# Kernel tuning notes

Hardware: AMD Instinct MI355X
Metric: run time of the kernel (lower is better)

Reference implementation:

```python
import jax, jax.numpy as jnp
import numpy as np

NUM_HEADS = 16
EMBED_DIM = 2048
HEAD_DIM = EMBED_DIM // NUM_HEADS        # 128
LATENT_DIM = HEAD_DIM // 4               # 32
GROUPS = HEAD_DIM // LATENT_DIM          # 4 latent sub-heads per q head
B, T = 1, 2048


def setup_inputs() -> dict:
    key = jax.random.key(0)
    ks = jax.random.split(key, 7)
    s_in = 1.0 / np.sqrt(EMBED_DIM)
    x = jax.random.normal(ks[0], (B, T, EMBED_DIM), dtype=jnp.float32)
    # torch Linear weights: [out_features, in_features]
    Wq = jax.random.normal(ks[1], (EMBED_DIM, EMBED_DIM), dtype=jnp.float32) * s_in
    Wk = jax.random.normal(ks[2], (EMBED_DIM, EMBED_DIM), dtype=jnp.float32) * s_in
    Wv = jax.random.normal(ks[3], (EMBED_DIM, EMBED_DIM), dtype=jnp.float32) * s_in
    Wlk = jax.random.normal(ks[4], (NUM_HEADS * LATENT_DIM, EMBED_DIM), dtype=jnp.float32) * s_in
    Wlv = jax.random.normal(ks[5], (NUM_HEADS * LATENT_DIM, EMBED_DIM), dtype=jnp.float32) * s_in
    Wo = jax.random.normal(ks[6], (EMBED_DIM, EMBED_DIM), dtype=jnp.float32) * s_in
    return {"x": x, "Wq": Wq, "Wk": Wk, "Wv": Wv, "Wlk": Wlk, "Wlv": Wlv, "Wo": Wo}


def reference(x, Wq, Wk, Wv, Wlk, Wlv, Wo):
    Bv, Tv, C = x.shape
    # q: [B,T,H,G,Dl]  (each head's 128-dim q split into 4 latent sub-heads)
    q = (x @ Wq.T).reshape(Bv, Tv, NUM_HEADS, GROUPS, LATENT_DIM)
    # latent k/v: [B,T,H,Dl], shared across the G sub-heads of each q head
    lk = (x @ Wlk.T).reshape(Bv, Tv, NUM_HEADS, LATENT_DIM)
    lv = (x @ Wlv.T).reshape(Bv, Tv, NUM_HEADS, LATENT_DIM)
    # k_proj / v_proj outputs are computed but unused in the original forward.
    scale = 1.0 / np.sqrt(HEAD_DIM).astype(np.float32)
    # scores: [B,H,G,T,T]
    scores = jnp.einsum('bthgd,bshd->bhgts', q, lk) * scale
    probs = jax.nn.softmax(scores, axis=-1)
    out = jnp.einsum('bhgts,bshd->bthgd', probs, lv).reshape(Bv, Tv, C)
    return out @ Wo.T
```

## Files before the change

kernel.cpp:

```cpp
#include <hip/hip_runtime.h>
#include <hip/hip_bf16.h>

typedef __bf16 bf16;
typedef __bf16 bf16x4 __attribute__((ext_vector_type(4)));
typedef __bf16 bf16x8 __attribute__((ext_vector_type(8)));
typedef float  f32x4  __attribute__((ext_vector_type(4)));

#define AS1 __attribute__((address_space(1)))
#define AS3 __attribute__((address_space(3)))

__device__ __forceinline__ void gload_lds16(const bf16* g, bf16* l) {
    __builtin_amdgcn_global_load_lds((const AS1 void*)g, (AS3 void*)l, 16, 0, 0);
}

__device__ __forceinline__ void stage8_f32(const float* s, bf16* l) {
    float4 a = *(const float4*)s;
    float4 b = *(const float4*)(s + 4);
    bf16x8 o;
    o[0] = (bf16)a.x; o[1] = (bf16)a.y; o[2] = (bf16)a.z; o[3] = (bf16)a.w;
    o[4] = (bf16)b.x; o[5] = (bf16)b.y; o[6] = (bf16)b.z; o[7] = (bf16)b.w;
    *(bf16x8*)l = o;
}

__device__ __forceinline__ void gemm_core64_k64(
    const bf16* __restrict__ A, const bf16* __restrict__ B,
    int m0, int n0, int K, f32x4 (&acc)[2][4],
    int wm, int r16, int q8)
{
    __shared__ __align__(16) bf16 As[2][128 * 64];
    __shared__ __align__(16) bf16 Bs[2][64 * 64];

    const int tid  = threadIdx.x;
    const int arow = tid >> 3;
    const int acol = ((tid & 7) ^ ((tid >> 3) & 7)) * 8;
    const int k7   = r16 & 7;

    auto stage = [&](int buf, int kt) {
#pragma unroll
        for (int j = 0; j < 4; ++j)
            gload_lds16(A + (size_t)(m0 + j * 32 + arow) * K + kt + acol,
                        &As[buf][(j * 256 + tid) * 8]);
#pragma unroll
        for (int j = 0; j < 2; ++j)
            gload_lds16(B + (size_t)(n0 + j * 32 + arow) * K + kt + acol,
                        &Bs[buf][(j * 256 + tid) * 8]);
    };

    stage(0, 0);
    __syncthreads();

    int cur = 0;
    for (int kt = 0; kt < K; kt += 64) {
        if (kt + 64 < K) stage(cur ^ 1, kt + 64);

        bf16x8 a[2][2], b[4][2];
#pragma unroll
        for (int r = 0; r < 2; ++r)
#pragma unroll
            for (int kc = 0; kc < 2; ++kc)
                a[r][kc] = *(const bf16x8*)&As[cur][(wm + r * 16 + r16) * 64
                                                   + ((kc * 4 + q8) ^ k7) * 8];
#pragma unroll
        for (int c = 0; c < 4; ++c)
#pragma unroll
            for (int kc = 0; kc < 2; ++kc)
                b[c][kc] = *(const bf16x8*)&Bs[cur][(c * 16 + r16) * 64
                                                   + ((kc * 4 + q8) ^ k7) * 8];
#pragma unroll
        for (int kc = 0; kc < 2; ++kc)
#pragma unroll
            for (int r = 0; r < 2; ++r)
#pragma unroll
                for (int c = 0; c < 4; ++c)
                    acc[r][c] = __builtin_amdgcn_mfma_f32_16x16x32_bf16(a[r][kc], b[c][kc], acc[r][c], 0, 0, 0);

        asm volatile("s_waitcnt vmcnt(0) lgkmcnt(0)" ::: "memory");
        __builtin_amdgcn_s_barrier();
        __builtin_amdgcn_sched_barrier(0);
        cur ^= 1;
    }
}

__global__ __launch_bounds__(256) void cvt4c(
    const float* __restrict__ s0, const float* __restrict__ s1,
    const float* __restrict__ s2, const float* __restrict__ s3,
    bf16* __restrict__ d0, bf16* __restrict__ d1, bf16* __restrict__ d2,
    bf16* __restrict__ d3)
{
    int bid = blockIdx.x;
    const float* S; bf16* D; int cb;
    if (bid < 2048)      { S = s0; D = d0; cb = bid; }
    else if (bid < 4096) { S = s1; D = d1; cb = bid - 2048; }
    else if (bid < 4608) { S = s2; D = d2; cb = bid - 4096; }
    else                 { S = s3; D = d3; cb = bid - 4608; }
    int off = (cb * 256 + threadIdx.x) * 8;
    stage8_f32(S + off, D + off);
}

__global__ __launch_bounds__(256) void proj_k64(
    const bf16* __restrict__ x, const bf16* __restrict__ Wq,
    const bf16* __restrict__ Wlk, const bf16* __restrict__ Wlv,
    bf16* __restrict__ Q, bf16* __restrict__ LK, bf16* __restrict__ LVt)
{
    const int hw  = blockIdx.x + 48 * blockIdx.y;
    const int xcd = hw & 7, c = hw >> 3;
    const int bx  = (xcd & 3) * 12 + c / 8;
    const int by  = (xcd >> 2) * 8 + (c & 7);

    const int tid = threadIdx.x, lane = tid & 63, wave = tid >> 6;
    const int wm = wave * 32;
    const int r16 = lane & 15, q8 = lane >> 4;
    f32x4 acc[2][4] = {};

    const bf16* Bv; int n0;
    if (bx < 32)      { Bv = Wq;  n0 = bx * 64; }
    else if (bx < 40) { Bv = Wlk; n0 = (bx - 32) * 64; }
    else              { Bv = Wlv; n0 = (bx - 40) * 64; }

    gemm_core64_k64(x, Bv, by * 128, n0, 2048, acc, wm, r16, q8);

    if (bx < 40) {
        bf16* C  = (bx < 32) ? Q : LK;
        int ldc  = (bx < 32) ? 2048 : 512;
        const float sc = (bx < 32) ? 0.08838834764831845f * 1.4426950408889634f : 1.0f;
#pragma unroll
        for (int r = 0; r < 2; ++r)
#pragma unroll
            for (int cc = 0; cc < 4; ++cc)
#pragma unroll
                for (int i = 0; i < 4; ++i) {
                    int row = by * 128 + wm + r * 16 + q8 * 4 + i;
                    int col = n0 + cc * 16 + r16;
                    C[(size_t)row * ldc + col] = (bf16)(acc[r][cc][i] * sc);
                }
    } else {
#pragma unroll
        for (int r = 0; r < 2; ++r)
#pragma unroll
            for (int cc = 0; cc < 4; ++cc) {
                int hd = n0 + cc * 16 + r16;
                int tb = by * 128 + wm + r * 16 + q8 * 4;
                bf16x4 pk;
#pragma unroll
                for (int i = 0; i < 4; ++i) pk[i] = (bf16)acc[r][cc][i];
                *(bf16x4*)&LVt[(size_t)hd * 2048 + tb] = pk;
            }
    }
}

__global__ __launch_bounds__(256) void out_k64(
    const bf16* __restrict__ A, const bf16* __restrict__ Wob, float* __restrict__ C)
{
    const int hw  = blockIdx.x + 32 * blockIdx.y;
    const int xcd = hw & 7, c = hw >> 3;
    const int bx  = (xcd & 3) * 8 + c / 8;
    const int by  = (xcd >> 2) * 8 + (c & 7);

    const int tid = threadIdx.x, lane = tid & 63, wave = tid >> 6;
    const int wm = wave * 32;
    const int r16 = lane & 15, q8 = lane >> 4;
    f32x4 acc[2][4] = {};
    gemm_core64_k64(A, Wob, by * 128, bx * 64, 2048, acc, wm, r16, q8);
#pragma unroll
    for (int r = 0; r < 2; ++r)
#pragma unroll
        for (int cc = 0; cc < 4; ++cc)
#pragma unroll
            for (int i = 0; i < 4; ++i) {
                int row = by * 128 + wm + r * 16 + q8 * 4 + i;
                int col = bx * 64 + cc * 16 + r16;
                C[(size_t)row * 2048 + col] = acc[r][cc][i];
            }
}

__global__ __launch_bounds__(256, 4) void attn7(
    const bf16* __restrict__ Q, const bf16* __restrict__ LK,
    const bf16* __restrict__ LVt, bf16* __restrict__ O,
    const float* __restrict__ Wo, bf16* __restrict__ Wob)
{
    __shared__ __align__(16) bf16 Ks[3][64 * 32];
    __shared__ __align__(16) bf16 Vs[3][32 * 64];
    __shared__ __align__(16) bf16 Ps[128 * 64];

    const int tid  = threadIdx.x;
    const int lane = tid & 63;
    const int w    = tid >> 6;
    const int r16  = lane & 15;
    const int q8   = lane >> 4;
    const int hg = blockIdx.y, h = hg >> 2, g = hg & 3;
    const int t0 = blockIdx.x * 128;

    bf16x8 qb[2];
#pragma unroll
    for (int p = 0; p < 2; ++p)
        qb[p] = *(const bf16x8*)(Q + (size_t)(t0 + w * 32 + p * 16 + r16) * 2048
                                 + h * 128 + g * 32 + q8 * 8);

    const int kr = tid >> 2;
    const int kq = (tid & 3) ^ ((tid >> 3) & 3);
    const bf16* kg = LK + (size_t)kr * 512 + h * 32 + kq * 8;
    const int vd = tid >> 3;
    const int vq = (tid & 7) ^ ((tid >> 3) & 7);
    const bf16* vg = LVt + (size_t)(h * 32 + vd) * 2048 + vq * 8;

    const int ksw = (r16 >> 1) & 3;
    const int vsw = r16 & 7;

    const int pk7 = r16 & 7;
    const int ph  = q8 >> 1;
    const int plo = (q8 & 1) * 4;
    const int pb0 = ((w * 2 + 0) * 16 + r16) * 64;
    const int pb1 = ((w * 2 + 1) * 16 + r16) * 64;

    bf16x8 ones;
#pragma unroll
    for (int j = 0; j < 8; ++j) ones[j] = (bf16)1.0f;

    f32x4 o_acc[2][2] = {};
    f32x4 l_acc[2] = {};
    const f32x4 z = {0.f, 0.f, 0.f, 0.f};

    gload_lds16(kg,                 &Ks[0][tid * 8]);
    gload_lds16(vg,                 &Vs[0][tid * 8]);
    gload_lds16(kg + (size_t)64 * 512, &Ks[1][tid * 8]);
    gload_lds16(vg + 64,               &Vs[1][tid * 8]);
    __syncthreads();

    int cur = 0, stg = 2;
    for (int sb = 0; sb < 2048; sb += 64) {
        const bool pf = (sb + 128 < 2048);
        if (pf) {
            gload_lds16(kg + (size_t)(sb + 128) * 512, &Ks[stg][tid * 8]);
            gload_lds16(vg + (sb + 128),               &Vs[stg][tid * 8]);
        }
        const bf16* ks = Ks[cur];
        const bf16* vs = Vs[cur];

        bf16x8 kb[4], vb[2][2];
#pragma unroll
        for (int cc = 0; cc < 4; ++cc)
            kb[cc] = *(const bf16x8*)&ks[(cc * 16 + r16) * 32 + (q8 ^ ksw) * 8];
#pragma unroll
        for (int kk = 0; kk < 2; ++kk)
#pragma unroll
            for (int ct = 0; ct < 2; ++ct)
                vb[kk][ct] = *(const bf16x8*)&vs[(ct * 16 + r16) * 64
                                                 + (((kk * 4 + q8) ^ vsw) * 8)];

#pragma unroll
        for (int p = 0; p < 2; ++p) {
            const int pbase = p ? pb1 : pb0;
            f32x4 sv[4];
            __builtin_amdgcn_s_setprio(1);
#pragma unroll
            for (int cc = 0; cc < 4; ++cc)
                sv[cc] = __builtin_amdgcn_mfma_f32_16x16x32_bf16(kb[cc], qb[p], z, 0, 0, 0);
            __builtin_amdgcn_s_setprio(0);
#pragma unroll
            for (int cc = 0; cc < 4; ++cc) {
                bf16x4 pkv;
#pragma unroll
                for (int i = 0; i < 4; ++i) pkv[i] = (bf16)exp2f(sv[cc][i]);
                *(bf16x4*)&Ps[pbase + ((cc * 2 + ph) ^ pk7) * 8 + plo] = pkv;
            }
        }

        __builtin_amdgcn_s_setprio(1);
#pragma unroll
        for (int p = 0; p < 2; ++p) {
            const int pbase = p ? pb1 : pb0;
#pragma unroll
            for (int kk = 0; kk < 2; ++kk) {
                bf16x8 ap = *(const bf16x8*)&Ps[pbase + ((kk * 4 + q8) ^ pk7) * 8];
#pragma unroll
                for (int ct = 0; ct < 2; ++ct)
                    o_acc[p][ct] = __builtin_amdgcn_mfma_f32_16x16x32_bf16(ap, vb[kk][ct], o_acc[p][ct], 0, 0, 0);
                l_acc[p] = __builtin_amdgcn_mfma_f32_16x16x32_bf16(ap, ones, l_acc[p], 0, 0, 0);
            }
        }
        __builtin_amdgcn_s_setprio(0);

        if (pf) asm volatile("s_waitcnt vmcnt(2) lgkmcnt(0)" ::: "memory");
        else    asm volatile("s_waitcnt vmcnt(0) lgkmcnt(0)" ::: "memory");
        __builtin_amdgcn_s_barrier();
        __builtin_amdgcn_sched_barrier(0);
        cur = (cur == 2) ? 0 : cur + 1;
        stg = (stg == 2) ? 0 : stg + 1;
    }

#pragma unroll
    for (int p = 0; p < 2; ++p)
#pragma unroll
        for (int i = 0; i < 4; ++i) {
            float inv = 1.0f / l_acc[p][i];
            int t = t0 + w * 32 + p * 16 + q8 * 4 + i;
#pragma unroll
            for (int ct = 0; ct < 2; ++ct) {
                int d = ct * 16 + r16;
                O[(size_t)t * 2048 + h * 128 + g * 32 + d] = (bf16)(o_acc[p][ct][i] * inv);
            }
        }

    {
        const int bid = blockIdx.y * 16 + blockIdx.x;
#pragma unroll
        for (int it = 0; it < 2; ++it) {
            size_t off = (size_t)bid * 4096 + (size_t)it * 2048 + (size_t)tid * 8;
            stage8_f32(Wo + off, Wob + off);
        }
    }
}

extern "C" void kernel_launch(void* const* d_in, const int* in_sizes, int n_in,
                              void* d_out, int out_size, void* d_ws, size_t ws_size,
                              hipStream_t stream) {
    const float* x   = (const float*)d_in[0];
    const float* Wq  = (const float*)d_in[1];
    const float* Wlk = (const float*)d_in[4];
    const float* Wlv = (const float*)d_in[5];
    const float* Wo  = (const float*)d_in[6];
    float* out = (float*)d_out;

    const size_t M4 = 4194304, M1 = 1048576;
    bf16* xb   = (bf16*)d_out;
    bf16* Wqb  = xb + M4;
    bf16* p    = (bf16*)d_ws;
    bf16* Wlkb = p; p += M1;
    bf16* Wlvb = p; p += M1;
    bf16* Wob  = p; p += M4;
    bf16* Qp   = p; p += M4;
    bf16* LKp  = p; p += M1;
    bf16* LVt  = p;
    bf16* ATT  = Qp;

    cvt4c<<<dim3(5120), 256, 0, stream>>>(x, Wq, Wlk, Wlv,
                                          xb, Wqb, Wlkb, Wlvb);
    proj_k64<<<dim3(48, 16), 256, 0, stream>>>(xb, Wqb, Wlkb, Wlvb,
                                               Qp, LKp, LVt);
    attn7<<<dim3(16, 64), 256, 0, stream>>>(Qp, LKp, LVt, ATT, Wo, Wob);
    out_k64<<<dim3(32, 16), 256, 0, stream>>>(ATT, Wob, out);
}
```

Baseline: 263.5 us.

## Fuse Q projection into attention kernel, shrink projection GEMM to latent K/V

The Q projection is moved out of the projection GEMM and computed inside each attention block as a 128x32 tile GEMM (x rows times the head-group slice of Wq), staged through shared memory and then used directly as the query fragment. This removes the write and re-read of the full Q tensor and lets the projection kernel handle only the latent K/V weights with a smaller grid. In exchange, each attention block now reads a 128x2048 slice of x, and the 16 attention blocks per row tile repeat that read, adding a long serial GEMM prologue before the attention loop. The K/V prefetch buffers are carved out of the same shared-memory array to keep occupancy.

```diff
diff --git a/kernel.cpp b/kernel.cpp
--- a/kernel.cpp
+++ b/kernel.cpp
@@ -97,32 +97,22 @@
     stage8_f32(S + off, D + off);
 }
 
-__global__ __launch_bounds__(256) void proj_k64(
-    const bf16* __restrict__ x, const bf16* __restrict__ Wq,
-    const bf16* __restrict__ Wlk, const bf16* __restrict__ Wlv,
-    bf16* __restrict__ Q, bf16* __restrict__ LK, bf16* __restrict__ LVt)
-{
-    const int hw  = blockIdx.x + 48 * blockIdx.y;
-    const int xcd = hw & 7, c = hw >> 3;
-    const int bx  = (xcd & 3) * 12 + c / 8;
-    const int by  = (xcd >> 2) * 8 + (c & 7);
-
+__global__ __launch_bounds__(256) void proj_lv(
+    const bf16* __restrict__ xb, const bf16* __restrict__ Wlk,
+    const bf16* __restrict__ Wlv, bf16* __restrict__ LK, bf16* __restrict__ LVt)
+{
+    const int bx = blockIdx.x, by = blockIdx.y;
     const int tid = threadIdx.x, lane = tid & 63, wave = tid >> 6;
     const int wm = wave * 32;
     const int r16 = lane & 15, q8 = lane >> 4;
     f32x4 acc[2][4] = {};
 
-    const bf16* Bv; int n0;
-    if (bx < 32)      { Bv = Wq;  n0 = bx * 64; }
-    else if (bx < 40) { Bv = Wlk; n0 = (bx - 32) * 64; }
-    else              { Bv = Wlv; n0 = (bx - 40) * 64; }
-
-    gemm_core64_k64(x, Bv, by * 128, n0, 2048, acc, wm, r16, q8);
-
-    if (bx < 40) {
-        bf16* C  = (bx < 32) ? Q : LK;
-        int ldc  = (bx < 32) ? 2048 : 512;
-        const float sc = (bx < 32) ? 0.08838834764831845f * 1.4426950408889634f : 1.0f;
+    const bf16* Bv = (bx < 8) ? Wlk : Wlv;
+    const int n0 = (bx & 7) * 64;
+
+    gemm_core64_k64(xb, Bv, by * 128, n0, 2048, acc, wm, r16, q8);
+
+    if (bx < 8) {
 #pragma unroll
         for (int r = 0; r < 2; ++r)
 #pragma unroll
@@ -131,7 +121,7 @@
                 for (int i = 0; i < 4; ++i) {
                     int row = by * 128 + wm + r * 16 + q8 * 4 + i;
                     int col = n0 + cc * 16 + r16;
-                    C[(size_t)row * ldc + col] = (bf16)(acc[r][cc][i] * sc);
+                    LK[(size_t)row * 512 + col] = (bf16)acc[r][cc][i];
                 }
     } else {
 #pragma unroll
@@ -173,14 +163,12 @@
             }
 }
 
-__global__ __launch_bounds__(256, 4) void attn7(
-    const bf16* __restrict__ Q, const bf16* __restrict__ LK,
-    const bf16* __restrict__ LVt, bf16* __restrict__ O,
-    const float* __restrict__ Wo, bf16* __restrict__ Wob)
-{
-    __shared__ __align__(16) bf16 Ks[3][64 * 32];
-    __shared__ __align__(16) bf16 Vs[3][32 * 64];
-    __shared__ __align__(16) bf16 Ps[128 * 64];
+__global__ __launch_bounds__(256, 4) void attn8(
+    const bf16* __restrict__ xb, const bf16* __restrict__ Wqb,
+    const bf16* __restrict__ LK, const bf16* __restrict__ LVt,
+    bf16* __restrict__ O, const float* __restrict__ Wo, bf16* __restrict__ Wob)
+{
+    __shared__ __align__(16) bf16 lds[20480];
 
     const int tid  = threadIdx.x;
     const int lane = tid & 63;
@@ -190,11 +178,81 @@
     const int hg = blockIdx.y, h = hg >> 2, g = hg & 3;
     const int t0 = blockIdx.x * 128;
 
+    {
+        bf16* As = lds;
+        bf16* Bs = lds + 16384;
+        const int arow = tid >> 3;
+        const int acol = ((tid & 7) ^ (arow & 7)) * 8;
+        const int k7   = r16 & 7;
+        f32x4 qacc[2][2] = {};
+
+        auto qstage = [&](int buf, int kt) {
+#pragma unroll
+            for (int j = 0; j < 4; ++j)
+                gload_lds16(xb + (size_t)(t0 + j * 32 + arow) * 2048 + kt + acol,
+                            &As[buf * 8192 + (j * 256 + tid) * 8]);
+            gload_lds16(Wqb + (size_t)(hg * 32 + arow) * 2048 + kt + acol,
+                        &Bs[buf * 2048 + tid * 8]);
+        };
+
+        qstage(0, 0);
+        __syncthreads();
+
+        int cur = 0;
+        for (int kt = 0; kt < 2048; kt += 64) {
+            if (kt + 64 < 2048) qstage(cur ^ 1, kt + 64);
+
+            bf16x8 a[2][2], b[2][2];
+#pragma unroll
+            for (int r = 0; r < 2; ++r)
+#pragma unroll
+                for (int kc = 0; kc < 2; ++kc)
+                    a[r][kc] = *(const bf16x8*)&As[cur * 8192
+                        + (w * 32 + r * 16 + r16) * 64 + ((kc * 4 + q8) ^ k7) * 8];
+#pragma unroll
+            for (int c = 0; c < 2; ++c)
+#pragma unroll
+                for (int kc = 0; kc < 2; ++kc)
+                    b[c][kc] = *(const bf16x8*)&Bs[cur * 2048
+                        + (c * 16 + r16) * 64 + ((kc * 4 + q8) ^ k7) * 8];
+#pragma unroll
+            for (int kc = 0; kc < 2; ++kc)
+#pragma unroll
+                for (int r = 0; r < 2; ++r)
+#pragma unroll
+                    for (int c = 0; c < 2; ++c)
+                        qacc[r][c] = __builtin_amdgcn_mfma_f32_16x16x32_bf16(a[r][kc], b[c][kc], qacc[r][c], 0, 0, 0);
+
+            asm volatile("s_waitcnt vmcnt(0) lgkmcnt(0)" ::: "memory");
+            __builtin_amdgcn_s_barrier();
+            __builtin_amdgcn_sched_barrier(0);
+            cur ^= 1;
+        }
+
+        bf16* Qtmp = lds;
+        const float Cc = 0.08838834764831845f * 1.4426950408889634f;
+#pragma unroll
+        for (int r = 0; r < 2; ++r)
+#pragma unroll
+            for (int c = 0; c < 2; ++c)
+#pragma unroll
+                for (int i = 0; i < 4; ++i)
+                    Qtmp[(w * 32 + r * 16 + q8 * 4 + i) * 32 + c * 16 + r16] =
+                        (bf16)(qacc[r][c][i] * Cc);
+        __syncthreads();
+    }
+
     bf16x8 qb[2];
 #pragma unroll
     for (int p = 0; p < 2; ++p)
-        qb[p] = *(const bf16x8*)(Q + (size_t)(t0 + w * 32 + p * 16 + r16) * 2048
-                                 + h * 128 + g * 32 + q8 * 8);
+        qb[p] = *(const bf16x8*)&lds[(w * 32 + p * 16 + r16) * 32 + q8 * 8];
+    asm volatile("s_waitcnt lgkmcnt(0)" ::: "memory");
+    __builtin_amdgcn_sched_barrier(0);
+    __syncthreads();
+
+    bf16* Ks = lds;
+    bf16* Vs = lds + 6144;
+    bf16* Ps = lds + 12288;
 
     const int kr = tid >> 2;
     const int kq = (tid & 3) ^ ((tid >> 3) & 3);
@@ -220,21 +278,21 @@
     f32x4 l_acc[2] = {};
     const f32x4 z = {0.f, 0.f, 0.f, 0.f};
 
-    gload_lds16(kg,                 &Ks[0][tid * 8]);
-    gload_lds16(vg,                 &Vs[0][tid * 8]);
-    gload_lds16(kg + (size_t)64 * 512, &Ks[1][tid * 8]);
-    gload_lds16(vg + 64,               &Vs[1][tid * 8]);
+    gload_lds16(kg,                    &Ks[0 * 2048 + tid * 8]);
+    gload_lds16(vg,                    &Vs[0 * 2048 + tid * 8]);
+    gload_lds16(kg + (size_t)64 * 512, &Ks[1 * 2048 + tid * 8]);
+    gload_lds16(vg + 64,               &Vs[1 * 2048 + tid * 8]);
     __syncthreads();
 
     int cur = 0, stg = 2;
     for (int sb = 0; sb < 2048; sb += 64) {
         const bool pf = (sb + 128 < 2048);
         if (pf) {
-            gload_lds16(kg + (size_t)(sb + 128) * 512, &Ks[stg][tid * 8]);
-            gload_lds16(vg + (sb + 128),               &Vs[stg][tid * 8]);
-        }
-        const bf16* ks = Ks[cur];
-        const bf16* vs = Vs[cur];
+            gload_lds16(kg + (size_t)(sb + 128) * 512, &Ks[stg * 2048 + tid * 8]);
+            gload_lds16(vg + (sb + 128),               &Vs[stg * 2048 + tid * 8]);
+        }
+        const bf16* ks = Ks + cur * 2048;
+        const bf16* vs = Vs + cur * 2048;
 
         bf16x8 kb[4], vb[2][2];
 #pragma unroll
@@ -328,15 +386,13 @@
     bf16* Wlkb = p; p += M1;
     bf16* Wlvb = p; p += M1;
     bf16* Wob  = p; p += M4;
-    bf16* Qp   = p; p += M4;
+    bf16* ATT  = p; p += M4;
     bf16* LKp  = p; p += M1;
     bf16* LVt  = p;
-    bf16* ATT  = Qp;
 
     cvt4c<<<dim3(5120), 256, 0, stream>>>(x, Wq, Wlk, Wlv,
                                           xb, Wqb, Wlkb, Wlvb);
-    proj_k64<<<dim3(48, 16), 256, 0, stream>>>(xb, Wqb, Wlkb, Wlvb,
-                                               Qp, LKp, LVt);
-    attn7<<<dim3(16, 64), 256, 0, stream>>>(Qp, LKp, LVt, ATT, Wo, Wob);
+    proj_lv<<<dim3(16, 16), 256, 0, stream>>>(xb, Wlkb, Wlvb, LKp, LVt);
+    attn8<<<dim3(16, 64), 256, 0, stream>>>(xb, Wqb, LKp, LVt, ATT, Wo, Wob);
     out_k64<<<dim3(32, 16), 256, 0, stream>>>(ATT, Wob, out);
 }
```

After: 280.4 us. 1.06x slower.
